# Performance work log

Measured on AMD Instinct MI355X. Metric: run time of the kernel, lower is better.

Reference implementation:

```python
import jax, jax.numpy as jnp
import numpy as np

D = 32
H = 64
B, N, M = 2, 512, 512


def setup_inputs() -> dict:
    key = jax.random.key(0)
    ks = jax.random.split(key, 6)
    s = 0.1  # modest init scale for MLP params
    return {
        "Q": jax.random.normal(ks[0], (B, N, D), dtype=jnp.float32),
        "K": jax.random.normal(ks[1], (B, M, D), dtype=jnp.float32),
        "w1": jax.random.normal(ks[2], (D, H), dtype=jnp.float32) * s,
        "b1": jax.random.normal(ks[3], (H,), dtype=jnp.float32) * s,
        "w2": jax.random.normal(ks[4], (H, D * D), dtype=jnp.float32) * s,
        "b2": jax.random.normal(ks[5], (D * D,), dtype=jnp.float32) * s,
    }


def _cholesky_factor(x, w1, b1, w2, b2):
    """L(x) with unit-ish softplus diagonal; x: [..., D] -> L: [..., D, D]."""
    h = jax.nn.silu(x @ w1 + b1)
    raw = h @ w2 + b2                      # [..., D*D]
    raw = 5.0 * jnp.tanh(raw / 5.0)        # soft clamp
    L = (raw + jnp.eye(D, dtype=x.dtype).reshape(-1)).reshape(x.shape[:-1] + (D, D))
    tril = jnp.tril(jnp.ones((D, D), dtype=x.dtype))
    diag = jnp.eye(D, dtype=x.dtype)
    L = L * tril
    L = L * (1.0 - diag) + (jax.nn.softplus(L) + 1e-4) * diag
    return L


def reference(Q, K, w1, b1, w2, b2):
    L_q = _cholesky_factor(Q, w1, b1, w2, b2)   # [B,N,D,D]
    L_k = _cholesky_factor(K, w1, b1, w2, b2)   # [B,M,D,D]
    delta = Q[:, :, None, :] - K[:, None, :, :]  # [B,N,M,D]
    # delta^T G_avg delta = 0.5 (||L_q^T delta||^2 + ||L_k^T delta||^2)
    vq = jnp.einsum('bnij,bnmi->bnmj', L_q, delta)  # L_q^T delta
    vk = jnp.einsum('bmij,bnmi->bnmj', L_k, delta)  # L_k^T delta
    dist_sq = 0.5 * (jnp.sum(vq * vq, axis=-1) + jnp.sum(vk * vk, axis=-1))
    return jnp.sqrt(jnp.clip(dist_sq, 1e-6, 1e6))
```

## Files before the change

### kernel.cpp

```cpp
#include <hip/hip_runtime.h>
#include <math.h>

namespace {
constexpr int KF  = 1152;
constexpr int RPB = 2;
}

typedef __bf16 v8bf __attribute__((ext_vector_type(8)));
typedef float  v4f  __attribute__((ext_vector_type(4)));

__device__ __forceinline__ unsigned short f2bf(float f) {
    union { float f; unsigned u; } v; v.f = f;
    unsigned r = v.u + 0x7FFFu + ((v.u >> 16) & 1u);
    return (unsigned short)(r >> 16);
}

__device__ __forceinline__ v8bf as_v8bf(uint4 u) {
    union { uint4 u; v8bf b; } c; c.u = u; return c.b;
}

__global__ __launch_bounds__(256, 4) void k_feat(
    const float* __restrict__ Q, const float* __restrict__ K,
    const float* __restrict__ w1, const float* __restrict__ b1,
    const float* __restrict__ w2, const float* __restrict__ b2,
    unsigned short* __restrict__ featA, unsigned short* __restrict__ featB,
    float* __restrict__ cOut)
{
    __shared__ __attribute__((aligned(16))) float x_s[RPB][32];
    __shared__ __attribute__((aligned(16))) float h_s[RPB][64];
    __shared__ __attribute__((aligned(16))) float L_s[RPB][32][36];
    __shared__ __attribute__((aligned(16))) float G_s[RPB][528];
    __shared__ __attribute__((aligned(16))) float u_s[RPB][32];
    __shared__ unsigned short tri_s[528];

    const int t  = threadIdx.x;
    const int g0 = blockIdx.x * RPB;

    for (int pr = t; pr < 528; pr += 256) {
        int j = (int)((65.0f - sqrtf(4225.0f - 8.0f * (float)pr)) * 0.5f);
        while (j > 0 && j * (65 - j) / 2 > pr) --j;
        while ((j + 1) * (64 - j) / 2 <= pr) ++j;
        int i = j + (pr - j * (65 - j) / 2);
        tri_s[pr] = (unsigned short)((i << 8) | j);
    }
    if (t < RPB * 32) {
        int r = t >> 5, i = t & 31;
        int g = g0 + r;
        const float* src = (g < 1024) ? (Q + (size_t)g * 32)
                                      : (K + (size_t)(g - 1024) * 32);
        x_s[r][i] = src[i];
    }
    __syncthreads();

    if (t < RPB * 64) {
        int r = t >> 6, j = t & 63;
        float z = b1[j];
        #pragma unroll
        for (int i = 0; i < 32; ++i) z = fmaf(x_s[r][i], w1[i * 64 + j], z);
        h_s[r][j] = z / (1.0f + __expf(-z));
    }
    __syncthreads();

    {
        const int p4 = t * 4;
        float acc[RPB][4];
        float4 bq = *(const float4*)&b2[p4];
        #pragma unroll
        for (int r = 0; r < RPB; ++r) {
            acc[r][0] = bq.x; acc[r][1] = bq.y; acc[r][2] = bq.z; acc[r][3] = bq.w;
        }
        #pragma unroll 1
        for (int jb = 0; jb < 8; ++jb) {
            float h8[RPB][8];
            #pragma unroll
            for (int r = 0; r < RPB; ++r) {
                *(float4*)&h8[r][0] = *(const float4*)&h_s[r][jb * 8 + 0];
                *(float4*)&h8[r][4] = *(const float4*)&h_s[r][jb * 8 + 4];
            }
            #pragma unroll
            for (int jj = 0; jj < 8; ++jj) {
                float4 w = *(const float4*)&w2[(size_t)(jb * 8 + jj) * 1024 + p4];
                #pragma unroll
                for (int r = 0; r < RPB; ++r) {
                    acc[r][0] = fmaf(h8[r][jj], w.x, acc[r][0]);
                    acc[r][1] = fmaf(h8[r][jj], w.y, acc[r][1]);
                    acc[r][2] = fmaf(h8[r][jj], w.z, acc[r][2]);
                    acc[r][3] = fmaf(h8[r][jj], w.w, acc[r][3]);
                }
            }
        }
        const int i  = p4 >> 5;
        const int j0 = p4 & 31;
        #pragma unroll
        for (int r = 0; r < RPB; ++r) {
            float4 lv;
            float* lvp = (float*)&lv;
            #pragma unroll
            for (int e = 0; e < 4; ++e) {
                int j = j0 + e;
                float raw = acc[r][e];
                float ex = __expf(0.4f * raw);
                float c5 = 5.0f * (ex - 1.0f) / (ex + 1.0f);
                float val;
                if (i < j)       val = 0.0f;
                else if (i == j) { float z = c5 + 1.0f; val = log1pf(__expf(z)) + 1e-4f; }
                else             val = c5;
                lvp[e] = val;
            }
            *(float4*)&L_s[r][i][j0] = lv;
        }
    }
    __syncthreads();

    for (int idx = t; idx < RPB * 528; idx += 256) {
        int r  = idx / 528;
        int pr = idx - r * 528;
        int tv = tri_s[pr];
        int i = tv >> 8, j = tv & 255;
        const float* Li = &L_s[r][i][0];
        const float* Lj = &L_s[r][j][0];
        float s = 0.0f;
        int nf = (j + 1) >> 2;
        for (int qq = 0; qq < nf; ++qq) {
            float4 a  = *(const float4*)&Li[qq * 4];
            float4 bb = *(const float4*)&Lj[qq * 4];
            s += a.x * bb.x + a.y * bb.y + a.z * bb.z + a.w * bb.w;
        }
        for (int tt = nf * 4; tt <= j; ++tt) s = fmaf(Li[tt], Lj[tt], s);
        G_s[r][pr] = s;
    }
    __syncthreads();

    if (t < RPB * 32) {
        int r = t >> 5, i = t & 31;
        float s = 0.0f;
        #pragma unroll
        for (int j = 0; j < 32; ++j) {
            float gv = (j <= i) ? G_s[r][j * (65 - j) / 2 + i - j]
                                : G_s[r][i * (65 - i) / 2 + j - i];
            s = fmaf(gv, x_s[r][j], s);
        }
        u_s[r][i] = s;
    }
    __syncthreads();

    if (t < RPB) {
        float s = 0.0f;
        #pragma unroll
        for (int i = 0; i < 32; ++i) s = fmaf(u_s[t][i], x_s[t][i], s);
        cOut[g0 + t] = s;
    }

    for (int idx = t; idx < RPB * (KF / 4); idx += 256) {
        int r   = idx / (KF / 4);
        int q   = idx - r * (KF / 4);
        int pos = q * 4;
        int g   = g0 + r;
        bool isA = (g < 1024);
        unsigned short* dst = isA ? (featA + (size_t)g * KF)
                                  : (featB + (size_t)(g - 1024) * KF);
        unsigned short ev[4];
        #pragma unroll
        for (int e = 0; e < 4; ++e) {
            int p = pos + e;
            float va;
            if (p < 1056) {
                int pr = (p < 528) ? p : p - 528;
                bool wantG = (p < 528) ? isA : !isA;
                int tv = tri_s[pr];
                int i = tv >> 8, j = tv & 255;
                float gv = G_s[r][pr] * ((i == j) ? 1.0f : 2.0f);
                float ov = x_s[r][i] * x_s[r][j];
                va = wantG ? gv : ov;
            } else if (p < 1088) {
                int i = p - 1056;
                va = isA ? u_s[r][i] : -2.0f * x_s[r][i];
            } else if (p < 1120) {
                int i = p - 1088;
                va = isA ? x_s[r][i] : -2.0f * u_s[r][i];
            } else {
                va = 0.0f;
            }
            ev[e] = f2bf(va);
        }
        uint2 w;
        w.x = (unsigned)ev[0] | ((unsigned)ev[1] << 16);
        w.y = (unsigned)ev[2] | ((unsigned)ev[3] << 16);
        *(uint2*)(dst + pos) = w;
    }
}

__global__ __launch_bounds__(64) void k_gemm(
    const unsigned short* __restrict__ featA,
    const unsigned short* __restrict__ featB,
    const float* __restrict__ cOut,
    float* __restrict__ out)
{
    const int lane = threadIdx.x;
    const int m0 = blockIdx.x * 32;
    const int n0 = blockIdx.y * 16;
    const int b  = blockIdx.z;
    const int fr = lane & 15;
    const int fq = lane >> 4;

    const unsigned short* pA0 = featA + (size_t)(b * 512 + n0 + fr) * KF + fq * 8;
    const unsigned short* pB0 = featB + (size_t)(b * 512 + m0 + fr) * KF + fq * 8;
    const unsigned short* pB1 = pB0 + (size_t)16 * KF;

    v4f acc00 = {0,0,0,0}, acc01 = {0,0,0,0};

    uint4 bA0[3], bB0[3], bB1[3];
    #pragma unroll
    for (int s = 0; s < 3; ++s) {
        bA0[s] = *(const uint4*)(pA0 + s * 32);
        bB0[s] = *(const uint4*)(pB0 + s * 32);
        bB1[s] = *(const uint4*)(pB1 + s * 32);
    }

    for (int ks = 0; ks < 36; ks += 3) {
        #pragma unroll
        for (int s = 0; s < 3; ++s) {
            v8bf a0  = as_v8bf(bA0[s]);
            v8bf b0v = as_v8bf(bB0[s]);
            v8bf b1v = as_v8bf(bB1[s]);
            int kn = ks + s + 3;
            if (kn < 36) {
                bA0[s] = *(const uint4*)(pA0 + kn * 32);
                bB0[s] = *(const uint4*)(pB0 + kn * 32);
                bB1[s] = *(const uint4*)(pB1 + kn * 32);
            }
            acc00 = __builtin_amdgcn_mfma_f32_16x16x32_bf16(a0, b0v, acc00, 0, 0, 0);
            acc01 = __builtin_amdgcn_mfma_f32_16x16x32_bf16(a0, b1v, acc01, 0, 0, 0);
        }
    }

    const int colm = lane & 15;
    const float cB_0 = cOut[1024 + b * 512 + m0 + colm];
    const float cB_1 = cOut[1024 + b * 512 + m0 + 16 + colm];
    const int rbase = lane >> 4;
    #pragma unroll
    for (int v = 0; v < 4; ++v) {
        int n = n0 + rbase * 4 + v;
        float cA = cOut[b * 512 + n];
        float d0 = 0.5f * (acc00[v] + cA + cB_0);
        float d1 = 0.5f * (acc01[v] + cA + cB_1);
        d0 = fminf(fmaxf(d0, 1e-6f), 1e6f);
        d1 = fminf(fmaxf(d1, 1e-6f), 1e6f);
        size_t base = ((size_t)(b * 512 + n)) * 512;
        out[base + m0 + colm]      = sqrtf(d0);
        out[base + m0 + 16 + colm] = sqrtf(d1);
    }
}

extern "C" void kernel_launch(void* const* d_in, const int* in_sizes, int n_in,
                              void* d_out, int out_size, void* d_ws, size_t ws_size,
                              hipStream_t stream)
{
    const float* Q  = (const float*)d_in[0];
    const float* K  = (const float*)d_in[1];
    const float* w1 = (const float*)d_in[2];
    const float* b1 = (const float*)d_in[3];
    const float* w2 = (const float*)d_in[4];
    const float* b2 = (const float*)d_in[5];
    float* out = (float*)d_out;

    unsigned short* featA = (unsigned short*)d_ws;
    unsigned short* featB = featA + (size_t)1024 * KF;
    float* cOut = (float*)(featB + (size_t)1024 * KF);

    k_feat<<<dim3(2048 / RPB), dim3(256), 0, stream>>>(Q, K, w1, b1, w2, b2, featA, featB, cOut);
    k_gemm<<<dim3(16, 32, 2), dim3(64), 0, stream>>>(featA, featB, cOut, out);
}
```

Before: 105.9 us.

## Split MLP into separate kernel with more rows per block for w2 reuse

The fused feature kernel is split in two. A new MLP kernel computes L for 4 rows per block, so each w2 load is reused across more rows, and writes L to workspace memory. A second kernel reloads L and does the Gram and feature work with 2 rows per block. This adds an extra launch and a global round trip for L (8 MB) in exchange for less w2 traffic and possibly higher occupancy in the feature kernel.

```diff
diff --git a/kernel.cpp b/kernel.cpp
--- a/kernel.cpp
+++ b/kernel.cpp
@@ -2,8 +2,9 @@
 #include <math.h>
 
 namespace {
-constexpr int KF  = 1152;
-constexpr int RPB = 2;
+constexpr int KF    = 1152;
+constexpr int RPB_M = 4;
+constexpr int RPB   = 2;
 }
 
 typedef __bf16 v8bf __attribute__((ext_vector_type(8)));
@@ -19,31 +20,19 @@
     union { uint4 u; v8bf b; } c; c.u = u; return c.b;
 }
 
-__global__ __launch_bounds__(256, 4) void k_feat(
+__global__ __launch_bounds__(256, 4) void k_mlp(
     const float* __restrict__ Q, const float* __restrict__ K,
     const float* __restrict__ w1, const float* __restrict__ b1,
     const float* __restrict__ w2, const float* __restrict__ b2,
-    unsigned short* __restrict__ featA, unsigned short* __restrict__ featB,
-    float* __restrict__ cOut)
+    float* __restrict__ L)
 {
-    __shared__ __attribute__((aligned(16))) float x_s[RPB][32];
-    __shared__ __attribute__((aligned(16))) float h_s[RPB][64];
-    __shared__ __attribute__((aligned(16))) float L_s[RPB][32][36];
-    __shared__ __attribute__((aligned(16))) float G_s[RPB][528];
-    __shared__ __attribute__((aligned(16))) float u_s[RPB][32];
-    __shared__ unsigned short tri_s[528];
+    __shared__ __attribute__((aligned(16))) float x_s[RPB_M][32];
+    __shared__ __attribute__((aligned(16))) float h_s[RPB_M][64];
 
     const int t  = threadIdx.x;
-    const int g0 = blockIdx.x * RPB;
-
-    for (int pr = t; pr < 528; pr += 256) {
-        int j = (int)((65.0f - sqrtf(4225.0f - 8.0f * (float)pr)) * 0.5f);
-        while (j > 0 && j * (65 - j) / 2 > pr) --j;
-        while ((j + 1) * (64 - j) / 2 <= pr) ++j;
-        int i = j + (pr - j * (65 - j) / 2);
-        tri_s[pr] = (unsigned short)((i << 8) | j);
-    }
-    if (t < RPB * 32) {
+    const int g0 = blockIdx.x * RPB_M;
+
+    if (t < RPB_M * 32) {
         int r = t >> 5, i = t & 31;
         int g = g0 + r;
         const float* src = (g < 1024) ? (Q + (size_t)g * 32)
@@ -52,7 +41,7 @@
     }
     __syncthreads();
 
-    if (t < RPB * 64) {
+    {
         int r = t >> 6, j = t & 63;
         float z = b1[j];
         #pragma unroll
@@ -63,17 +52,17 @@
 
     {
         const int p4 = t * 4;
-        float acc[RPB][4];
+        float acc[RPB_M][4];
         float4 bq = *(const float4*)&b2[p4];
         #pragma unroll
-        for (int r = 0; r < RPB; ++r) {
+        for (int r = 0; r < RPB_M; ++r) {
             acc[r][0] = bq.x; acc[r][1] = bq.y; acc[r][2] = bq.z; acc[r][3] = bq.w;
         }
         #pragma unroll 1
         for (int jb = 0; jb < 8; ++jb) {
-            float h8[RPB][8];
+            float h8[RPB_M][8];
             #pragma unroll
-            for (int r = 0; r < RPB; ++r) {
+            for (int r = 0; r < RPB_M; ++r) {
                 *(float4*)&h8[r][0] = *(const float4*)&h_s[r][jb * 8 + 0];
                 *(float4*)&h8[r][4] = *(const float4*)&h_s[r][jb * 8 + 4];
             }
@@ -81,7 +70,7 @@
             for (int jj = 0; jj < 8; ++jj) {
                 float4 w = *(const float4*)&w2[(size_t)(jb * 8 + jj) * 1024 + p4];
                 #pragma unroll
-                for (int r = 0; r < RPB; ++r) {
+                for (int r = 0; r < RPB_M; ++r) {
                     acc[r][0] = fmaf(h8[r][jj], w.x, acc[r][0]);
                     acc[r][1] = fmaf(h8[r][jj], w.y, acc[r][1]);
                     acc[r][2] = fmaf(h8[r][jj], w.z, acc[r][2]);
@@ -92,7 +81,7 @@
         const int i  = p4 >> 5;
         const int j0 = p4 & 31;
         #pragma unroll
-        for (int r = 0; r < RPB; ++r) {
+        for (int r = 0; r < RPB_M; ++r) {
             float4 lv;
             float* lvp = (float*)&lv;
             #pragma unroll
@@ -107,8 +96,47 @@
                 else             val = c5;
                 lvp[e] = val;
             }
-            *(float4*)&L_s[r][i][j0] = lv;
-        }
+            *(float4*)&L[(size_t)(g0 + r) * 1024 + p4] = lv;
+        }
+    }
+}
+
+__global__ __launch_bounds__(256, 6) void k_feat2(
+    const float* __restrict__ Q, const float* __restrict__ K,
+    const float* __restrict__ L,
+    unsigned short* __restrict__ featA, unsigned short* __restrict__ featB,
+    float* __restrict__ cOut)
+{
+    __shared__ __attribute__((aligned(16))) float x_s[RPB][32];
+    __shared__ __attribute__((aligned(16))) float L_s[RPB][32][36];
+    __shared__ __attribute__((aligned(16))) float G_s[RPB][528];
+    __shared__ __attribute__((aligned(16))) float u_s[RPB][32];
+    __shared__ unsigned short tri_s[528];
+
+    const int t  = threadIdx.x;
+    const int g0 = blockIdx.x * RPB;
+
+    for (int pr = t; pr < 528; pr += 256) {
+        int j = (int)((65.0f - sqrtf(4225.0f - 8.0f * (float)pr)) * 0.5f);
+        while (j > 0 && j * (65 - j) / 2 > pr) --j;
+        while ((j + 1) * (64 - j) / 2 <= pr) ++j;
+        int i = j + (pr - j * (65 - j) / 2);
+        tri_s[pr] = (unsigned short)((i << 8) | j);
+    }
+    if (t < RPB * 32) {
+        int r = t >> 5, i = t & 31;
+        int g = g0 + r;
+        const float* src = (g < 1024) ? (Q + (size_t)g * 32)
+                                      : (K + (size_t)(g - 1024) * 32);
+        x_s[r][i] = src[i];
+    }
+    for (int idx = t; idx < RPB * 256; idx += 256) {
+        int r  = idx >> 8;
+        int e  = idx & 255;
+        int i  = e >> 3;
+        int j0 = (e & 7) << 2;
+        *(float4*)&L_s[r][i][j0] =
+            *(const float4*)&L[(size_t)(g0 + r) * 1024 + i * 32 + j0];
     }
     __syncthreads();
 
@@ -267,7 +295,9 @@
     unsigned short* featA = (unsigned short*)d_ws;
     unsigned short* featB = featA + (size_t)1024 * KF;
     float* cOut = (float*)(featB + (size_t)1024 * KF);
-
-    k_feat<<<dim3(2048 / RPB), dim3(256), 0, stream>>>(Q, K, w1, b1, w2, b2, featA, featB, cOut);
-    k_gemm<<<dim3(16, 32, 2), dim3(64), 0, stream>>>(featA, featB, cOut, out);
-}
+    float* L    = cOut + 2048;
+
+    k_mlp  <<<dim3(2048 / RPB_M), dim3(256), 0, stream>>>(Q, K, w1, b1, w2, b2, L);
+    k_feat2<<<dim3(2048 / RPB),   dim3(256), 0, stream>>>(Q, K, L, featA, featB, cOut);
+    k_gemm <<<dim3(16, 32, 2),    dim3(64),  0, stream>>>(featA, featB, cOut, out);
+}
```

New measurement: 110.7 us. 4.5% more time.
